# Optimization experiments

Measured on AMD Instinct MI355X. Metric: run time of the kernel, lower is better.

The kernel has to match this reference:

```python
import jax, jax.numpy as jnp
import numpy as np

D, H, HKV, HD = 1024, 16, 4, 64
GQ = H // HKV           # query heads per kv head (gqa_groups)
BS, STRIDE, TB, WIN = 32, 16, 16, 512
NEG = -1e9
EPS = 1e-5


def _ln(x, w, b):
    m = x.mean(-1, keepdims=True)
    v = ((x - m) ** 2).mean(-1, keepdims=True)
    return (x - m) * jax.lax.rsqrt(v + EPS) * w + b


def setup_inputs():
    key = jax.random.key(0)
    ks = jax.random.split(key, 20)
    B, S = 2, 2048
    w = lambda k, s: jax.random.normal(k, s, jnp.float32) * 0.02
    return dict(
        x=jax.random.normal(ks[0], (B, S, D), jnp.float32),
        ln1_w=jnp.ones((D,), jnp.float32), ln1_b=jnp.zeros((D,), jnp.float32),
        wq=w(ks[1], (D, H * HD)), bq=jnp.zeros((H * HD,), jnp.float32),
        wk=w(ks[2], (D, HKV * HD)), bk=jnp.zeros((HKV * HD,), jnp.float32),
        wv=w(ks[3], (D, HKV * HD)), bv=jnp.zeros((HKV * HD,), jnp.float32),
        wg=w(ks[4], (D, 3 * H)), bg=jnp.zeros((3 * H,), jnp.float32),
        wo=w(ks[5], (H * HD, D)), bo=jnp.zeros((D,), jnp.float32),
        ln2_w=jnp.ones((D,), jnp.float32), ln2_b=jnp.zeros((D,), jnp.float32),
        w1=w(ks[6], (D, 4 * D)), b1=jnp.zeros((4 * D,), jnp.float32),
        w2=w(ks[7], (4 * D, D)), b2=jnp.zeros((D,), jnp.float32),
    )


def _forward(x, ln1_w, ln1_b, wq, bq, wk, bk, wv, bv, wg, bg, wo, bo,
             ln2_w, ln2_b, w1, b1, w2, b2):
    B, S, _ = x.shape
    nb = S // BS
    h = _ln(x, ln1_w, ln1_b)
    q = (h @ wq + bq).reshape(B, S, H, HD).transpose(0, 2, 1, 3)    # [B,H,S,hd]
    k = (h @ wk + bk).reshape(B, S, HKV, HD).transpose(0, 2, 1, 3)  # [B,Hkv,S,hd]
    v = (h @ wv + bv).reshape(B, S, HKV, HD).transpose(0, 2, 1, 3)
    qg = q.reshape(B, HKV, GQ, S, HD)          # group queries by kv head
    qb = qg.reshape(B, HKV, GQ, nb, BS, HD)    # query blocks
    scale = HD ** -0.5

    # ---- branch 1: compressed attention (overlapping block pooling, stride)
    nc = (S - BS) // STRIDE + 1
    cidx = jnp.arange(nc)[:, None] * STRIDE + jnp.arange(BS)[None, :]
    ck = k[:, :, cidx].mean(axis=3)            # [B,Hkv,nc,hd]
    cv = v[:, :, cidx].mean(axis=3)
    cend = jnp.arange(nc) * STRIDE + BS - 1
    cmask = jnp.arange(S)[:, None] >= cend[None, :]   # [S,nc] causal at block end
    cs = jnp.where(cmask, jnp.einsum('bkgsd,bknd->bkgsn', qg, ck) * scale, NEG)
    oc = jnp.einsum('bkgsn,bknd->bkgsd', jax.nn.softmax(cs, axis=-1), cv)
    oc = jnp.where(cmask.any(-1)[:, None], oc, 0.0)   # zero rows with no visible block

    # ---- branch 2: top-k selected-block attention (selection per query block, per GQA group)
    kbm = k.reshape(B, HKV, nb, BS, HD).mean(3)       # pooled key blocks
    qbm = qb.mean(4)                                  # pooled query blocks
    imp = jnp.einsum('bkgnd,bkmd->bknm', qbm, kbm)    # importance, summed over group heads
    causal_blk = jnp.arange(nb)[:, None] >= jnp.arange(nb)[None, :]
    imp = jnp.where(causal_blk, imp, NEG)
    imp = jnp.where(jnp.eye(nb, dtype=bool), 1e9, imp)  # always keep current block
    _, sel = jax.lax.top_k(imp, TB)                     # [B,Hkv,nb,TB]
    L = TB * BS
    sel_pos = (sel[..., None] * BS + jnp.arange(BS)).reshape(B, HKV, nb, L)
    flat = sel_pos.reshape(B, HKV, nb * L)[..., None]
    sk = jnp.take_along_axis(k, flat, axis=2).reshape(B, HKV, nb, L, HD)
    sv = jnp.take_along_axis(v, flat, axis=2).reshape(B, HKV, nb, L, HD)
    qpos = (jnp.arange(nb) * BS)[:, None] + jnp.arange(BS)            # [nb,BS]
    smask = sel_pos[:, :, :, None, :] <= qpos[None, None, :, :, None]  # [B,Hkv,nb,BS,L]
    ss = jnp.where(smask[:, :, None],
                   jnp.einsum('bkgnqd,bknld->bkgnql', qb, sk) * scale, NEG)
    os_ = jnp.einsum('bkgnql,bknld->bkgnqd', jax.nn.softmax(ss, axis=-1), sv)
    os_ = os_.reshape(B, HKV, GQ, S, HD)

    # ---- branch 3: sliding-window attention (blocked gather, no dense SxS)
    widx = (jnp.arange(nb) * BS)[:, None] + jnp.arange(-WIN, BS)[None, :]
    wmask = (widx[:, None, :] >= 0) & (widx[:, None, :] <= qpos[..., None])
    widxc = jnp.clip(widx, 0, S - 1)
    wk_ = k[:, :, widxc]
    wv_ = v[:, :, widxc]
    ws = jnp.where(wmask, jnp.einsum('bkgnqd,bknwd->bkgnqw', qb, wk_) * scale, NEG)
    ow = jnp.einsum('bkgnqw,bknwd->bkgnqd', jax.nn.softmax(ws, axis=-1), wv_)
    ow = ow.reshape(B, HKV, GQ, S, HD)

    # ---- gated combination + output projection
    g = jax.nn.sigmoid(h @ wg + bg).reshape(B, S, H, 3).transpose(0, 2, 1, 3)  # [B,H,S,3]
    att = (g[..., 0:1] * oc.reshape(B, H, S, HD)
           + g[..., 1:2] * os_.reshape(B, H, S, HD)
           + g[..., 2:3] * ow.reshape(B, H, S, HD))
    att = att.transpose(0, 2, 1, 3).reshape(B, S, H * HD) @ wo + bo
    x1 = x + att

    # ---- dense FFN (use_moe=False): Linear -> GELU -> Linear, residual
    h2 = _ln(x1, ln2_w, ln2_b)
    return x1 + jax.nn.gelu(h2 @ w1 + b1, approximate=False) @ w2 + b2


def reference(x, ln1_w, ln1_b, wq, bq, wk, bk, wv, bv, wg, bg, wo, bo,
              ln2_w, ln2_b, w1, b1, w2, b2):
    return _forward(x, ln1_w, ln1_b, wq, bq, wk, bk, wv, bv, wg, bg, wo, bo,
                    ln2_w, ln2_b, w1, b1, w2, b2)
```

## Files before the change

### kernel.cpp

```cpp
#include <hip/hip_runtime.h>
#include <hip/hip_bf16.h>
#include <math.h>

typedef __hip_bfloat16 bft;
typedef __attribute__((ext_vector_type(8))) short bf16x8;
typedef __attribute__((ext_vector_type(4))) float f32x4;

constexpr int cB = 2, cS = 2048, cD = 1024, cH = 16, cHKV = 4, cGQ = 4, cHD = 64;
constexpr int cBS = 32, cTB = 16, cNB = 64, cNC = 127;

#define GL16(gp, lp) __builtin_amdgcn_global_load_lds((const __attribute__((address_space(1))) void*)(gp), (__attribute__((address_space(3))) void*)(lp), 16, 0, 0)
#define FENCE asm volatile("" ::: "memory")

__device__ __forceinline__ float bf2f(short h) {
    return __uint_as_float(((unsigned int)(unsigned short)h) << 16);
}

__global__ void k_transpose_cvt(const float* __restrict__ src, bft* __restrict__ dst, int K, int N) {
    __shared__ float tile[32][33];
    int kb = blockIdx.x * 32, nb = blockIdx.y * 32;
    int tx = threadIdx.x, ty = threadIdx.y;
    #pragma unroll
    for (int i = 0; i < 32; i += 8) {
        int k = kb + ty + i, n = nb + tx;
        tile[ty + i][tx] = (k < K && n < N) ? src[(size_t)k * N + n] : 0.f;
    }
    __syncthreads();
    #pragma unroll
    for (int i = 0; i < 32; i += 8) {
        int n = nb + ty + i, k = kb + tx;
        if (n < N && k < K) dst[(size_t)n * K + k] = __float2bfloat16(tile[tx][ty + i]);
    }
}

__global__ __launch_bounds__(256) void k_ln(const float* __restrict__ src, const float* __restrict__ w,
                                            const float* __restrict__ b, bft* __restrict__ dst) {
    int row = blockIdx.x; int t = threadIdx.x;
    const float4* xr = (const float4*)(src + (size_t)row * cD);
    float4 v = xr[t];
    float s = v.x + v.y + v.z + v.w;
    #pragma unroll
    for (int o = 32; o; o >>= 1) s += __shfl_xor(s, o);
    __shared__ float red[8];
    int wid = t >> 6, lane = t & 63;
    if (lane == 0) red[wid] = s;
    __syncthreads();
    float mean = (red[0] + red[1] + red[2] + red[3]) * (1.f / cD);
    float dx = v.x - mean, dy = v.y - mean, dz = v.z - mean, dw = v.w - mean;
    float sq = dx * dx + dy * dy + dz * dz + dw * dw;
    #pragma unroll
    for (int o = 32; o; o >>= 1) sq += __shfl_xor(sq, o);
    if (lane == 0) red[4 + wid] = sq;
    __syncthreads();
    float var = (red[4] + red[5] + red[6] + red[7]) * (1.f / cD);
    float rstd = rsqrtf(var + 1e-5f);
    float4 wv = ((const float4*)w)[t];
    float4 bv = ((const float4*)b)[t];
    bft* o_ = dst + (size_t)row * cD + t * 4;
    o_[0] = __float2bfloat16(dx * rstd * wv.x + bv.x);
    o_[1] = __float2bfloat16(dy * rstd * wv.y + bv.y);
    o_[2] = __float2bfloat16(dz * rstd * wv.z + bv.z);
    o_[3] = __float2bfloat16(dw * rstd * wv.w + bv.w);
}

template<int MODE>
__global__ __launch_bounds__(256) void k_gemm(const bft* __restrict__ A, const bft* __restrict__ Bt,
        int M, int N, int K,
        const float* __restrict__ bias, const float* __restrict__ add,
        float* __restrict__ outf, bft* __restrict__ outb,
        float* __restrict__ oq, float* __restrict__ okk, float* __restrict__ ovv, float* __restrict__ og,
        const float* __restrict__ bq, const float* __restrict__ bk,
        const float* __restrict__ bv, const float* __restrict__ bg,
        bft* __restrict__ oqb) {
    __shared__ __align__(16) bft As[128 * 64];
    __shared__ __align__(16) bft Bs[128 * 64];
    int tid = threadIdx.x;
    int nwg = gridDim.x * gridDim.y;
    int bid = blockIdx.y * gridDim.x + blockIdx.x;
    int q8 = nwg >> 3;
    int wg = (bid & 7) * q8 + (bid >> 3);
    int bx = wg % gridDim.x, by = wg / gridDim.x;
    int m0 = by * 128, n0 = bx * 128;
    int lane = tid & 63, wid = tid >> 6;
    int wr = wid >> 1, wc = wid & 1;
    int lrow = lane & 15, lk = lane >> 4;
    f32x4 acc[4][4];
    #pragma unroll
    for (int i = 0; i < 4; ++i)
        #pragma unroll
        for (int j = 0; j < 4; ++j) acc[i][j] = (f32x4)0.f;

    for (int kt = 0; kt < K; kt += 64) {
        #pragma unroll
        for (int sh = 0; sh < 4; ++sh) {
            int p = sh * 256 + tid;
            int row = p >> 3;
            int slot = p & 7;
            int ss = slot ^ (row & 7);
            const bft* ga = A + (size_t)(m0 + row) * K + kt + ss * 8;
            const bft* gb = Bt + (size_t)(n0 + row) * K + kt + ss * 8;
            GL16(ga, (char*)As + p * 16);
            GL16(gb, (char*)Bs + p * 16);
        }
        __syncthreads();
        #pragma unroll
        for (int kh = 0; kh < 2; ++kh) {
            bf16x8 af[4], bfv[4];
            #pragma unroll
            for (int mi = 0; mi < 4; ++mi) {
                int row = wr * 64 + mi * 16 + lrow;
                int c8 = kh * 4 + lk;
                af[mi] = *(const bf16x8*)((const char*)As + row * 128 + ((c8 ^ (row & 7)) * 16));
            }
            #pragma unroll
            for (int ni = 0; ni < 4; ++ni) {
                int row = wc * 64 + ni * 16 + lrow;
                int c8 = kh * 4 + lk;
                bfv[ni] = *(const bf16x8*)((const char*)Bs + row * 128 + ((c8 ^ (row & 7)) * 16));
            }
            #pragma unroll
            for (int mi = 0; mi < 4; ++mi)
                #pragma unroll
                for (int ni = 0; ni < 4; ++ni)
                    acc[mi][ni] = __builtin_amdgcn_mfma_f32_16x16x32_bf16(af[mi], bfv[ni], acc[mi][ni], 0, 0, 0);
        }
        __syncthreads();
    }
    #pragma unroll
    for (int mi = 0; mi < 4; ++mi)
        #pragma unroll
        for (int ni = 0; ni < 4; ++ni)
            #pragma unroll
            for (int r = 0; r < 4; ++r) {
                int gr = m0 + wr * 64 + mi * 16 + lk * 4 + r;
                int gc = n0 + wc * 64 + ni * 16 + lrow;
                float val = acc[mi][ni][r];
                if (MODE == 0) {
                    if (gc < 1024) {
                        float qv2 = val + bq[gc];
                        oq[(size_t)gr * 1024 + gc] = qv2;
                        oqb[(size_t)gr * 1024 + gc] = __float2bfloat16(qv2 * 0.125f);
                    }
                    else if (gc < 1280) okk[(size_t)gr * 256 + gc - 1024] = val + bk[gc - 1024];
                    else if (gc < 1536) ovv[(size_t)gr * 256 + gc - 1280] = val + bv[gc - 1280];
                    else if (gc < 1584) {
                        float t2 = val + bg[gc - 1536];
                        og[(size_t)gr * 48 + gc - 1536] = 1.f / (1.f + __expf(-t2));
                    }
                } else if (MODE == 1) {
                    size_t o = (size_t)gr * N + gc;
                    outf[o] = val + bias[gc] + add[o];
                } else if (MODE == 2) {
                    float t2 = val + bias[gc];
                    float ge = 0.5f * t2 * (1.f + erff(t2 * 0.70710678118654752f));
                    outb[(size_t)gr * N + gc] = __float2bfloat16(ge);
                } else {
                    size_t o = (size_t)gr * N + gc;
                    outf[o] = val + bias[gc] + add[o];
                }
            }
}

__global__ __launch_bounds__(512) void k_gemm256_gelu(const bft* __restrict__ A, const bft* __restrict__ Bt,
                                                      const float* __restrict__ bias, bft* __restrict__ outb) {
    constexpr int K = 1024, N = 4096, NT = K / 64;
    __shared__ __align__(16) bft As[2][256 * 64];
    __shared__ __align__(16) bft Bs[2][256 * 64];
    int tid = threadIdx.x;
    int nwg = gridDim.x * gridDim.y;
    int bid = blockIdx.y * gridDim.x + blockIdx.x;
    int q8 = nwg >> 3;
    int wg = (bid & 7) * q8 + (bid >> 3);
    int bx = wg % gridDim.x, by = wg / gridDim.x;
    int m0 = by * 256, n0 = bx * 256;
    int w = tid >> 6, lane = tid & 63, lrow = lane & 15, lk = lane >> 4;
    int wr = w >> 2, wc = w & 3;
    int l8 = lane >> 3, l7 = lane & 7;
    int ssrc = (l7 ^ l8) * 8;

    auto stageA = [&](int buf, int h, int kt) {
        int rbase = 32 * w + 16 * h;
        const bft* g0 = A + (size_t)(m0 + rbase + l8) * K + kt + ssrc;
        GL16(g0, (char*)As[buf] + rbase * 128 + lane * 16);
        const bft* g1 = A + (size_t)(m0 + rbase + 8 + l8) * K + kt + ssrc;
        GL16(g1, (char*)As[buf] + rbase * 128 + 1024 + lane * 16);
    };
    auto stageB = [&](int buf, int h, int kt) {
        int rbase = 32 * w + 16 * h;
        const bft* g0 = Bt + (size_t)(n0 + rbase + l8) * K + kt + ssrc;
        GL16(g0, (char*)Bs[buf] + rbase * 128 + lane * 16);
        const bft* g1 = Bt + (size_t)(n0 + rbase + 8 + l8) * K + kt + ssrc;
        GL16(g1, (char*)Bs[buf] + rbase * 128 + 1024 + lane * 16);
    };
    auto ldA = [&](int buf, int mi, int kk) {
        int r = wr * 128 + mi * 16 + lrow;
        return *(const bf16x8*)((const char*)As[buf] + r * 128 + (((kk * 4 + lk) ^ (r & 7)) * 16));
    };
    auto ldB = [&](int buf, int ni, int kk) {
        int r = wc * 64 + ni * 16 + lrow;
        return *(const bf16x8*)((const char*)Bs[buf] + r * 128 + (((kk * 4 + lk) ^ (r & 7)) * 16));
    };

    f32x4 acc[8][4];
    #pragma unroll
    for (int i = 0; i < 8; ++i)
        #pragma unroll
        for (int j = 0; j < 4; ++j) acc[i][j] = (f32x4)0.f;

    stageA(0, 0, 0); stageB(0, 0, 0); stageA(0, 1, 0); stageB(0, 1, 0);
    asm volatile("s_waitcnt vmcnt(4)" ::: "memory");
    FENCE; __builtin_amdgcn_s_barrier(); FENCE;

    bf16x8 aE[4][2], aO[4][2], bE[2][2], bO[2][2];
    for (int t = 0; t < NT; ++t) {
        int cur = t & 1, nxt = cur ^ 1;
        int ktn = (t + 1) * 64;
        bool pre = (t + 1 < NT);
        #pragma unroll
        for (int i = 0; i < 4; ++i)
            #pragma unroll
            for (int kk = 0; kk < 2; ++kk) aE[i][kk] = ldA(cur, 2 * i, kk);
        #pragma unroll
        for (int j = 0; j < 2; ++j)
            #pragma unroll
            for (int kk = 0; kk < 2; ++kk) bE[j][kk] = ldB(cur, 2 * j, kk);
        if (pre) { stageA(nxt, 0, ktn); asm volatile("s_waitcnt vmcnt(2)" ::: "memory"); }
        else     {                       asm volatile("s_waitcnt vmcnt(0)" ::: "memory"); }
        FENCE; __builtin_amdgcn_s_barrier(); FENCE;
        __builtin_amdgcn_s_setprio(1);
        #pragma unroll
        for (int i = 0; i < 4; ++i)
            #pragma unroll
            for (int j = 0; j < 2; ++j)
                #pragma unroll
                for (int kk = 0; kk < 2; ++kk)
                    acc[2 * i][2 * j] = __builtin_amdgcn_mfma_f32_16x16x32_bf16(aE[i][kk], bE[j][kk], acc[2 * i][2 * j], 0, 0, 0);
        __builtin_amdgcn_s_setprio(0);
        FENCE; __builtin_amdgcn_s_barrier(); FENCE;
        #pragma unroll
        for (int j = 0; j < 2; ++j)
            #pragma unroll
            for (int kk = 0; kk < 2; ++kk) bO[j][kk] = ldB(cur, 2 * j + 1, kk);
        if (pre) stageB(nxt, 0, ktn);
        FENCE; __builtin_amdgcn_s_barrier(); FENCE;
        __builtin_amdgcn_s_setprio(1);
        #pragma unroll
        for (int i = 0; i < 4; ++i)
            #pragma unroll
            for (int j = 0; j < 2; ++j)
                #pragma unroll
                for (int kk = 0; kk < 2; ++kk)
                    acc[2 * i][2 * j + 1] = __builtin_amdgcn_mfma_f32_16x16x32_bf16(aE[i][kk], bO[j][kk], acc[2 * i][2 * j + 1], 0, 0, 0);
        __builtin_amdgcn_s_setprio(0);
        FENCE; __builtin_amdgcn_s_barrier(); FENCE;
        #pragma unroll
        for (int i = 0; i < 4; ++i)
            #pragma unroll
            for (int kk = 0; kk < 2; ++kk) aO[i][kk] = ldA(cur, 2 * i + 1, kk);
        if (pre) stageA(nxt, 1, ktn);
        FENCE; __builtin_amdgcn_s_barrier(); FENCE;
        __builtin_amdgcn_s_setprio(1);
        #pragma unroll
        for (int i = 0; i < 4; ++i)
            #pragma unroll
            for (int j = 0; j < 2; ++j)
                #pragma unroll
                for (int kk = 0; kk < 2; ++kk)
                    acc[2 * i + 1][2 * j] = __builtin_amdgcn_mfma_f32_16x16x32_bf16(aO[i][kk], bE[j][kk], acc[2 * i + 1][2 * j], 0, 0, 0);
        __builtin_amdgcn_s_setprio(0);
        FENCE; __builtin_amdgcn_s_barrier(); FENCE;
        if (pre) { stageB(nxt, 1, ktn); asm volatile("s_waitcnt vmcnt(4)" ::: "memory"); }
        FENCE; __builtin_amdgcn_s_barrier(); FENCE;
        __builtin_amdgcn_s_setprio(1);
        #pragma unroll
        for (int i = 0; i < 4; ++i)
            #pragma unroll
            for (int j = 0; j < 2; ++j)
                #pragma unroll
                for (int kk = 0; kk < 2; ++kk)
                    acc[2 * i + 1][2 * j + 1] = __builtin_amdgcn_mfma_f32_16x16x32_bf16(aO[i][kk], bO[j][kk], acc[2 * i + 1][2 * j + 1], 0, 0, 0);
        __builtin_amdgcn_s_setprio(0);
        FENCE; __builtin_amdgcn_s_barrier(); FENCE;
    }
    #pragma unroll
    for (int mi = 0; mi < 8; ++mi)
        #pragma unroll
        for (int ni = 0; ni < 4; ++ni)
            #pragma unroll
            for (int r = 0; r < 4; ++r) {
                int gr = m0 + wr * 128 + mi * 16 + lk * 4 + r;
                int gc = n0 + wc * 64 + ni * 16 + lrow;
                float t2 = acc[mi][ni][r] + bias[gc];
                float ge = 0.5f * t2 * (1.f + erff(t2 * 0.70710678118654752f));
                outb[(size_t)gr * N + gc] = __float2bfloat16(ge);
            }
}

__global__ __launch_bounds__(512) void k_gemm256_sk(const bft* __restrict__ A, const bft* __restrict__ Bt,
                                                    bft* __restrict__ q0, bft* __restrict__ q1,
                                                    bft* __restrict__ q2, bft* __restrict__ q3) {
    constexpr int KT = 4096, N = 1024, NT = 16;
    __shared__ __align__(16) bft As[2][256 * 64];
    __shared__ __align__(16) bft Bs[2][256 * 64];
    int tid = threadIdx.x;
    int flat = blockIdx.x;
    int wg = (flat & 7) * 32 + (flat >> 3);
    int slice = wg >> 6; int rem = wg & 63;
    int m0 = (rem >> 2) * 256, n0 = (rem & 3) * 256;
    int kbase = slice * 1024;
    int w = tid >> 6, lane = tid & 63, lrow = lane & 15, lk = lane >> 4;
    int wr = w >> 2, wc = w & 3;
    int l8 = lane >> 3, l7 = lane & 7;
    int ssrc = (l7 ^ l8) * 8;

    auto stageA = [&](int buf, int h, int kt) {
        int rbase = 32 * w + 16 * h;
        const bft* g0 = A + (size_t)(m0 + rbase + l8) * KT + kbase + kt + ssrc;
        GL16(g0, (char*)As[buf] + rbase * 128 + lane * 16);
        const bft* g1 = A + (size_t)(m0 + rbase + 8 + l8) * KT + kbase + kt + ssrc;
        GL16(g1, (char*)As[buf] + rbase * 128 + 1024 + lane * 16);
    };
    auto stageB = [&](int buf, int h, int kt) {
        int rbase = 32 * w + 16 * h;
        const bft* g0 = Bt + (size_t)(n0 + rbase + l8) * KT + kbase + kt + ssrc;
        GL16(g0, (char*)Bs[buf] + rbase * 128 + lane * 16);
        const bft* g1 = Bt + (size_t)(n0 + rbase + 8 + l8) * KT + kbase + kt + ssrc;
        GL16(g1, (char*)Bs[buf] + rbase * 128 + 1024 + lane * 16);
    };
    auto ldA = [&](int buf, int mi, int kk) {
        int r = wr * 128 + mi * 16 + lrow;
        return *(const bf16x8*)((const char*)As[buf] + r * 128 + (((kk * 4 + lk) ^ (r & 7)) * 16));
    };
    auto ldB = [&](int buf, int ni, int kk) {
        int r = wc * 64 + ni * 16 + lrow;
        return *(const bf16x8*)((const char*)Bs[buf] + r * 128 + (((kk * 4 + lk) ^ (r & 7)) * 16));
    };

    f32x4 acc[8][4];
    #pragma unroll
    for (int i = 0; i < 8; ++i)
        #pragma unroll
        for (int j = 0; j < 4; ++j) acc[i][j] = (f32x4)0.f;

    stageA(0, 0, 0); stageB(0, 0, 0); stageA(0, 1, 0); stageB(0, 1, 0);
    asm volatile("s_waitcnt vmcnt(4)" ::: "memory");
    FENCE; __builtin_amdgcn_s_barrier(); FENCE;

    bf16x8 aE[4][2], aO[4][2], bE[2][2], bO[2][2];
    for (int t = 0; t < NT; ++t) {
        int cur = t & 1, nxt = cur ^ 1;
        int ktn = (t + 1) * 64;
        bool pre = (t + 1 < NT);
        #pragma unroll
        for (int i = 0; i < 4; ++i)
            #pragma unroll
            for (int kk = 0; kk < 2; ++kk) aE[i][kk] = ldA(cur, 2 * i, kk);
        #pragma unroll
        for (int j = 0; j < 2; ++j)
            #pragma unroll
            for (int kk = 0; kk < 2; ++kk) bE[j][kk] = ldB(cur, 2 * j, kk);
        if (pre) { stageA(nxt, 0, ktn); asm volatile("s_waitcnt vmcnt(2)" ::: "memory"); }
        else     {                       asm volatile("s_waitcnt vmcnt(0)" ::: "memory"); }
        FENCE; __builtin_amdgcn_s_barrier(); FENCE;
        __builtin_amdgcn_s_setprio(1);
        #pragma unroll
        for (int i = 0; i < 4; ++i)
            #pragma unroll
            for (int j = 0; j < 2; ++j)
                #pragma unroll
                for (int kk = 0; kk < 2; ++kk)
                    acc[2 * i][2 * j] = __builtin_amdgcn_mfma_f32_16x16x32_bf16(aE[i][kk], bE[j][kk], acc[2 * i][2 * j], 0, 0, 0);
        __builtin_amdgcn_s_setprio(0);
        FENCE; __builtin_amdgcn_s_barrier(); FENCE;
        #pragma unroll
        for (int j = 0; j < 2; ++j)
            #pragma unroll
            for (int kk = 0; kk < 2; ++kk) bO[j][kk] = ldB(cur, 2 * j + 1, kk);
        if (pre) stageB(nxt, 0, ktn);
        FENCE; __builtin_amdgcn_s_barrier(); FENCE;
        __builtin_amdgcn_s_setprio(1);
        #pragma unroll
        for (int i = 0; i < 4; ++i)
            #pragma unroll
            for (int j = 0; j < 2; ++j)
                #pragma unroll
                for (int kk = 0; kk < 2; ++kk)
                    acc[2 * i][2 * j + 1] = __builtin_amdgcn_mfma_f32_16x16x32_bf16(aE[i][kk], bO[j][kk], acc[2 * i][2 * j + 1], 0, 0, 0);
        __builtin_amdgcn_s_setprio(0);
        FENCE; __builtin_amdgcn_s_barrier(); FENCE;
        #pragma unroll
        for (int i = 0; i < 4; ++i)
            #pragma unroll
            for (int kk = 0; kk < 2; ++kk) aO[i][kk] = ldA(cur, 2 * i + 1, kk);
        if (pre) stageA(nxt, 1, ktn);
        FENCE; __builtin_amdgcn_s_barrier(); FENCE;
        __builtin_amdgcn_s_setprio(1);
        #pragma unroll
        for (int i = 0; i < 4; ++i)
            #pragma unroll
            for (int j = 0; j < 2; ++j)
                #pragma unroll
                for (int kk = 0; kk < 2; ++kk)
                    acc[2 * i + 1][2 * j] = __builtin_amdgcn_mfma_f32_16x16x32_bf16(aO[i][kk], bE[j][kk], acc[2 * i + 1][2 * j], 0, 0, 0);
        __builtin_amdgcn_s_setprio(0);
        FENCE; __builtin_amdgcn_s_barrier(); FENCE;
        if (pre) { stageB(nxt, 1, ktn); asm volatile("s_waitcnt vmcnt(4)" ::: "memory"); }
        FENCE; __builtin_amdgcn_s_barrier(); FENCE;
        __builtin_amdgcn_s_setprio(1);
        #pragma unroll
        for (int i = 0; i < 4; ++i)
            #pragma unroll
            for (int j = 0; j < 2; ++j)
                #pragma unroll
                for (int kk = 0; kk < 2; ++kk)
                    acc[2 * i + 1][2 * j + 1] = __builtin_amdgcn_mfma_f32_16x16x32_bf16(aO[i][kk], bO[j][kk], acc[2 * i + 1][2 * j + 1], 0, 0, 0);
        __builtin_amdgcn_s_setprio(0);
        FENCE; __builtin_amdgcn_s_barrier(); FENCE;
    }
    bft* pp = (slice == 0) ? q0 : (slice == 1) ? q1 : (slice == 2) ? q2 : q3;
    #pragma unroll
    for (int mi = 0; mi < 8; ++mi)
        #pragma unroll
        for (int ni = 0; ni < 4; ++ni)
            #pragma unroll
            for (int r = 0; r < 4; ++r) {
                int gr = m0 + wr * 128 + mi * 16 + lk * 4 + r;
                int gc = n0 + wc * 64 + ni * 16 + lrow;
                pp[(size_t)gr * N + gc] = __float2bfloat16(acc[mi][ni][r]);
            }
}

__global__ __launch_bounds__(256) void k_mlpred(const bft* __restrict__ q0, const bft* __restrict__ q1,
                                                const bft* __restrict__ q2, const bft* __restrict__ q3,
                                                const float* __restrict__ x1, const float* __restrict__ b2,
                                                float* __restrict__ out) {
    size_t i = ((size_t)blockIdx.x * 256 + threadIdx.x) * 8;
    bf16x8 a0 = *(const bf16x8*)(q0 + i);
    bf16x8 a1 = *(const bf16x8*)(q1 + i);
    bf16x8 a2 = *(const bf16x8*)(q2 + i);
    bf16x8 a3 = *(const bf16x8*)(q3 + i);
    int col = (int)(i & 1023);
    float4 b0 = *(const float4*)(b2 + col);
    float4 b1v = *(const float4*)(b2 + col + 4);
    float4 x0 = *(const float4*)(x1 + i);
    float4 x1v = *(const float4*)(x1 + i + 4);
    float s[8];
    #pragma unroll
    for (int j = 0; j < 8; ++j)
        s[j] = bf2f(a0[j]) + bf2f(a1[j]) + bf2f(a2[j]) + bf2f(a3[j]);
    float4 o0 = make_float4(s[0] + b0.x + x0.x, s[1] + b0.y + x0.y, s[2] + b0.z + x0.z, s[3] + b0.w + x0.w);
    float4 o1 = make_float4(s[4] + b1v.x + x1v.x, s[5] + b1v.y + x1v.y, s[6] + b1v.z + x1v.z, s[7] + b1v.w + x1v.w);
    *(float4*)(out + i) = o0;
    *(float4*)(out + i + 4) = o1;
}

__global__ __launch_bounds__(64) void k_cmp_kv(const float* __restrict__ k, const float* __restrict__ v,
                                               bft* __restrict__ ck, bft* __restrict__ cvT) {
    int idx = blockIdx.x;
    int n = idx & 127; int bk = idx >> 7; int kv = bk & 3; int b = bk >> 2;
    int d = threadIdx.x;
    if (n == 127) {
        ck[(size_t)bk * 8192 + 127 * 64 + d] = __float2bfloat16(0.f);
        cvT[(size_t)bk * 8192 + d * 128 + 127] = __float2bfloat16(0.f);
        return;
    }
    float sk = 0.f, sv = 0.f;
    int base = b * cS + n * 16;
    for (int j = 0; j < cBS; ++j) {
        size_t o = (size_t)(base + j) * 256 + kv * 64 + d;
        sk += k[o]; sv += v[o];
    }
    ck[(size_t)bk * 8192 + n * 64 + d] = __float2bfloat16(sk * (1.f / 32.f));
    cvT[(size_t)bk * 8192 + d * 128 + n] = __float2bfloat16(sv * (1.f / 32.f));
}

__global__ __launch_bounds__(256) void k_cmp_attn(const float* __restrict__ q, const bft* __restrict__ ck,
                                                  const bft* __restrict__ cvT, const float* __restrict__ gates,
                                                  float* __restrict__ att) {
    __shared__ __align__(16) bft Qs[256 * 64];
    __shared__ __align__(16) bft Ks[128 * 64];
    __shared__ __align__(16) bft VTs[64 * 128];
    __shared__ __align__(16) bft Ps[4 * 16 * 128];
    int idx = blockIdx.x;
    int chunk = idx & 31; int bk = idx >> 5; int kv = bk & 3; int b = bk >> 2;
    int tid = threadIdx.x;
    {
        int r = tid; int h = r >> 6, toff = r & 63;
        const float4* src = (const float4*)(q + ((size_t)(b * cS + chunk * 64 + toff)) * 1024 + (kv * 4 + h) * 64);
        #pragma unroll
        for (int s = 0; s < 8; ++s) {
            float4 a = src[2 * s], c = src[2 * s + 1];
            bf16x8 pk;
            bft* pe = (bft*)&pk;
            pe[0] = __float2bfloat16(a.x); pe[1] = __float2bfloat16(a.y);
            pe[2] = __float2bfloat16(a.z); pe[3] = __float2bfloat16(a.w);
            pe[4] = __float2bfloat16(c.x); pe[5] = __float2bfloat16(c.y);
            pe[6] = __float2bfloat16(c.z); pe[7] = __float2bfloat16(c.w);
            *(bf16x8*)((char*)Qs + r * 128 + ((s ^ (r & 7)) * 16)) = pk;
        }
    }
    if (tid < 128) {
        int r = tid;
        const bf16x8* src = (const bf16x8*)(ck + (size_t)bk * 8192 + r * 64);
        #pragma unroll
        for (int s = 0; s < 8; ++s)
            *(bf16x8*)((char*)Ks + r * 128 + ((s ^ (r & 7)) * 16)) = src[s];
    }
    if (tid < 64) {
        int r = tid;
        const bf16x8* src = (const bf16x8*)(cvT + (size_t)bk * 8192 + r * 128);
        #pragma unroll
        for (int s = 0; s < 16; ++s)
            *(bf16x8*)((char*)VTs + r * 256 + ((s ^ (r & 7)) * 16)) = src[s];
    }
    __syncthreads();

    int w = tid >> 6, lane = tid & 63, lrow = lane & 15, lk = lane >> 4;
    int hg = kv * cGQ + w;
    #pragma unroll
    for (int rt = 0; rt < 4; ++rt) {
        int rowb = w * 64 + rt * 16;
        bf16x8 aq[2];
        #pragma unroll
        for (int kh = 0; kh < 2; ++kh) {
            int r = rowb + lrow;
            aq[kh] = *(const bf16x8*)((const char*)Qs + r * 128 + (((kh * 4 + lk) ^ (r & 7)) * 16));
        }
        f32x4 sa[8];
        #pragma unroll
        for (int nt = 0; nt < 8; ++nt) {
            sa[nt] = (f32x4)0.f;
            #pragma unroll
            for (int kh = 0; kh < 2; ++kh) {
                int kr = nt * 16 + lrow;
                bf16x8 bv_ = *(const bf16x8*)((const char*)Ks + kr * 128 + (((kh * 4 + lk) ^ (kr & 7)) * 16));
                sa[nt] = __builtin_amdgcn_mfma_f32_16x16x32_bf16(aq[kh], bv_, sa[nt], 0, 0, 0);
            }
        }
        float mrow[4], srow[4]; int nv[4];
        #pragma unroll
        for (int r = 0; r < 4; ++r) {
            int s_abs = chunk * 64 + rt * 16 + lk * 4 + r;
            nv[r] = (s_abs >= 31) ? (((s_abs - 31) >> 4) + 1) : 0;
            mrow[r] = -INFINITY; srow[r] = 0.f;
        }
        #pragma unroll
        for (int nt = 0; nt < 8; ++nt) {
            int key = nt * 16 + lrow;
            #pragma unroll
            for (int r = 0; r < 4; ++r) {
                float sc = sa[nt][r] * 0.125f;
                if (key < nv[r]) mrow[r] = fmaxf(mrow[r], sc);
            }
        }
        #pragma unroll
        for (int r = 0; r < 4; ++r) {
            #pragma unroll
            for (int o = 8; o; o >>= 1) mrow[r] = fmaxf(mrow[r], __shfl_xor(mrow[r], o));
        }
        #pragma unroll
        for (int nt = 0; nt < 8; ++nt) {
            int key = nt * 16 + lrow;
            #pragma unroll
            for (int r = 0; r < 4; ++r) {
                float sc = sa[nt][r] * 0.125f;
                float p = (key < nv[r]) ? __expf(sc - mrow[r]) : 0.f;
                srow[r] += p;
                int rit = lk * 4 + r;
                *(bft*)((char*)Ps + w * 4096 + rit * 256 + ((((key >> 3) ^ (rit & 7))) * 16) + (key & 7) * 2) =
                    __float2bfloat16(p);
            }
        }
        #pragma unroll
        for (int r = 0; r < 4; ++r) {
            #pragma unroll
            for (int o = 8; o; o >>= 1) srow[r] += __shfl_xor(srow[r], o);
        }
        f32x4 oa[4];
        #pragma unroll
        for (int dt = 0; dt < 4; ++dt) oa[dt] = (f32x4)0.f;
        #pragma unroll
        for (int kc = 0; kc < 4; ++kc) {
            bf16x8 pa = *(const bf16x8*)((const char*)Ps + w * 4096 + lrow * 256 + (((kc * 4 + lk) ^ (lrow & 7)) * 16));
            #pragma unroll
            for (int dt = 0; dt < 4; ++dt) {
                int vr = dt * 16 + lrow;
                bf16x8 vb = *(const bf16x8*)((const char*)VTs + vr * 256 + (((kc * 4 + lk) ^ (vr & 7)) * 16));
                oa[dt] = __builtin_amdgcn_mfma_f32_16x16x32_bf16(pa, vb, oa[dt], 0, 0, 0);
            }
        }
        float inv[4]; int toks[4];
        #pragma unroll
        for (int r = 0; r < 4; ++r) {
            int tok = chunk * 64 + rt * 16 + lk * 4 + r;
            toks[r] = tok;
            float g0 = gates[((size_t)(b * cS + tok)) * 48 + hg * 3 + 0];
            inv[r] = (srow[r] > 0.f) ? (g0 / srow[r]) : 0.f;
        }
        #pragma unroll
        for (int dt = 0; dt < 4; ++dt)
            #pragma unroll
            for (int r = 0; r < 4; ++r)
                att[((size_t)(b * cS + toks[r])) * 1024 + hg * 64 + dt * 16 + lrow] = oa[dt][r] * inv[r];
    }
}

__global__ __launch_bounds__(256) void k_kvprep(const float* __restrict__ k, const float* __restrict__ v,
                                                bft* __restrict__ kb16, bft* __restrict__ vT16) {
    __shared__ float vt[64 * 65];
    int idx = blockIdx.x; int tc = idx & 31; int kv = (idx >> 5) & 3; int b = idx >> 7;
    int t = threadIdx.x; int ti = t >> 2, seg = t & 3, d0 = seg * 16;
    const float4* ks = (const float4*)(k + (size_t)(b * cS + tc * 64 + ti) * 256 + kv * 64 + d0);
    const float4* vs = (const float4*)(v + (size_t)(b * cS + tc * 64 + ti) * 256 + kv * 64 + d0);
    bft* kd = kb16 + ((size_t)(b * 4 + kv) * 2048 + tc * 64 + ti) * 64 + d0;
    #pragma unroll
    for (int i = 0; i < 4; ++i) {
        float4 a = ks[i];
        kd[i * 4 + 0] = __float2bfloat16(a.x); kd[i * 4 + 1] = __float2bfloat16(a.y);
        kd[i * 4 + 2] = __float2bfloat16(a.z); kd[i * 4 + 3] = __float2bfloat16(a.w);
        float4 c = vs[i];
        vt[ti * 65 + d0 + i * 4 + 0] = c.x; vt[ti * 65 + d0 + i * 4 + 1] = c.y;
        vt[ti * 65 + d0 + i * 4 + 2] = c.z; vt[ti * 65 + d0 + i * 4 + 3] = c.w;
    }
    __syncthreads();
    int d = t >> 2, ts0 = (t & 3) * 16;
    bft* vd = vT16 + ((size_t)(b * 4 + kv) * 64 + d) * 2048 + tc * 64 + ts0;
    #pragma unroll
    for (int i = 0; i < 16; ++i) vd[i] = __float2bfloat16(vt[(ts0 + i) * 65 + d]);
}

__global__ __launch_bounds__(256) void k_selwin(const bft* __restrict__ qb16, const bft* __restrict__ kb16,
                                                const bft* __restrict__ vT16, const int* __restrict__ sel,
                                                const float* __restrict__ gates, const float* __restrict__ attb,
                                                bft* __restrict__ att16) {
    __shared__ __align__(16) bft Qs[128 * 64];
    __shared__ __align__(16) bft Ks[3][32 * 64];
    __shared__ __align__(16) bft Vs[3][64 * 32];
    __shared__ __align__(16) bft Ps[4][32 * 32];
    __shared__ int msL[40];
    __shared__ int nmS[2];
    int idx = blockIdx.x;
    int n = idx & 63; int kv = (idx >> 6) & 3; int b = idx >> 8;
    int bkv = b * 4 + kv;
    int tid = threadIdx.x;
    int w = tid >> 6, lane = tid & 63, lrow = lane & 15, lk = lane >> 4;
    int h = kv * 4 + w;

    #pragma unroll
    for (int c = 0; c < 4; ++c) {
        int p = c * 256 + tid; int r = p >> 3, s = p & 7;
        const bft* src = qb16 + ((size_t)(b * cS + n * 32 + (r & 31))) * 1024 + (kv * 4 + (r >> 5)) * 64 + ((s ^ (r & 7)) * 8);
        GL16(src, (char*)Qs + p * 16);
    }
    {
        int p = tid; int row = p >> 3, s = p & 7;
        const bft* srck = kb16 + ((size_t)bkv * 2048 + n * 32 + row) * 64 + ((s ^ (row & 7)) * 8);
        GL16(srck, (char*)Ks[0] + p * 16);
        int rowv = p >> 2, g3 = p & 3;
        const bft* srcv = vT16 + ((size_t)bkv * 64 + rowv) * 2048 + n * 32 + ((g3 ^ (rowv & 3)) * 8);
        GL16(srcv, (char*)Vs[0] + p * 16);
    }
    if (tid == 0) {
        const int* selp = sel + ((size_t)bkv * cNB + n) * cTB;
        int nm = 0;
        #pragma unroll
        for (int t = 0; t < cTB; ++t) { int m = selp[t]; if (m <= n) msL[nm++] = m; }
        nmS[0] = nm;
        int m0 = (n > 16) ? (n - 16) : 0;
        for (int m = m0; m <= n; ++m) msL[nm++] = m;
        nmS[1] = nm;
    }
    asm volatile("s_waitcnt vmcnt(0)" ::: "memory");
    FENCE; __builtin_amdgcn_s_barrier(); FENCE;

    int p1 = nmS[0], nm = nmS[1];
    bf16x8 qf[2][2];
    #pragma unroll
    for (int qt = 0; qt < 2; ++qt)
        #pragma unroll
        for (int kh = 0; kh < 2; ++kh) {
            int r = w * 32 + qt * 16 + lrow;
            qf[qt][kh] = *(const bf16x8*)((const char*)Qs + r * 128 + (((kh * 4 + lk) ^ (r & 7)) * 16));
        }

    f32x4 oa[2][4], accf[2][4];
    float sacc[2] = {0.f, 0.f};
    #pragma unroll
    for (int qt = 0; qt < 2; ++qt)
        #pragma unroll
        for (int dt = 0; dt < 4; ++dt) { oa[qt][dt] = (f32x4)0.f; accf[qt][dt] = (f32x4)0.f; }

    for (int i = 0; i < nm; ++i) {
        int buf = i % 3;
        if (i == 0 && nm > 1) {
            int m1 = msL[1];
            int p = tid; int row = p >> 3, s = p & 7;
            const bft* srck = kb16 + ((size_t)bkv * 2048 + m1 * 32 + row) * 64 + ((s ^ (row & 7)) * 8);
            GL16(srck, (char*)Ks[1] + p * 16);
            int rowv = p >> 2, g3 = p & 3;
            const bft* srcv = vT16 + ((size_t)bkv * 64 + rowv) * 2048 + m1 * 32 + ((g3 ^ (rowv & 3)) * 8);
            GL16(srcv, (char*)Vs[1] + p * 16);
        }
        if (i + 2 < nm) {
            int m2 = msL[i + 2]; int sl = (i + 2) % 3;
            int p = tid; int row = p >> 3, s = p & 7;
            const bft* srck = kb16 + ((size_t)bkv * 2048 + m2 * 32 + row) * 64 + ((s ^ (row & 7)) * 8);
            GL16(srck, (char*)Ks[sl] + p * 16);
            int rowv = p >> 2, g3 = p & 3;
            const bft* srcv = vT16 + ((size_t)bkv * 64 + rowv) * 2048 + m2 * 32 + ((g3 ^ (rowv & 3)) * 8);
            GL16(srcv, (char*)Vs[sl] + p * 16);
        }
        int m = msL[i];
        bool diag = (m == n);
        #pragma unroll
        for (int qt = 0; qt < 2; ++qt) {
            int q = qt * 16 + lrow;
            #pragma unroll
            for (int kt = 0; kt < 2; ++kt) {
                f32x4 a = (f32x4)0.f;
                #pragma unroll
                for (int kh = 0; kh < 2; ++kh) {
                    int kr = kt * 16 + lrow;
                    bf16x8 ak = *(const bf16x8*)((const char*)Ks[buf] + kr * 128 + (((kh * 4 + lk) ^ (kr & 7)) * 16));
                    a = __builtin_amdgcn_mfma_f32_16x16x32_bf16(ak, qf[qt][kh], a, 0, 0, 0);
                }
                int k0 = kt * 16 + lk * 4;
                float p0 = (!diag || k0 <= q)     ? __expf(a[0]) : 0.f;
                float p1v = (!diag || k0 + 1 <= q) ? __expf(a[1]) : 0.f;
                float p2 = (!diag || k0 + 2 <= q) ? __expf(a[2]) : 0.f;
                float p3 = (!diag || k0 + 3 <= q) ? __expf(a[3]) : 0.f;
                sacc[qt] += p0 + p1v + p2 + p3;
                bft h0 = __float2bfloat16(p0), h1 = __float2bfloat16(p1v);
                bft h2 = __float2bfloat16(p2), h3 = __float2bfloat16(p3);
                unsigned int w0 = ((unsigned int)(*(unsigned short*)&h1) << 16) | (unsigned int)(*(unsigned short*)&h0);
                unsigned int w1 = ((unsigned int)(*(unsigned short*)&h3) << 16) | (unsigned int)(*(unsigned short*)&h2);
                int g = kt * 2 + (lk >> 1);
                *(uint2*)((char*)Ps[w] + q * 64 + ((g ^ (q & 3)) * 16) + (lk & 1) * 8) = make_uint2(w0, w1);
            }
        }
        #pragma unroll
        for (int qt = 0; qt < 2; ++qt) {
            int q = qt * 16 + lrow;
            bf16x8 pa = *(const bf16x8*)((const char*)Ps[w] + q * 64 + ((lk ^ (q & 3)) * 16));
            #pragma unroll
            for (int dt = 0; dt < 4; ++dt) {
                int vr = dt * 16 + lrow;
                bf16x8 vb = *(const bf16x8*)((const char*)Vs[buf] + vr * 64 + ((lk ^ (vr & 3)) * 16));
                oa[qt][dt] = __builtin_amdgcn_mfma_f32_16x16x32_bf16(pa, vb, oa[qt][dt], 0, 0, 0);
            }
        }
        if (i == p1 - 1 || i == nm - 1) {
            int gi = (i == p1 - 1) ? 1 : 2;
            #pragma unroll
            for (int qt = 0; qt < 2; ++qt) {
                float s2 = sacc[qt];
                s2 += __shfl_xor(s2, 16); s2 += __shfl_xor(s2, 32);
                #pragma unroll
                for (int r = 0; r < 4; ++r) {
                    float l = __shfl(s2, lk * 4 + r);
                    int tok = n * 32 + qt * 16 + lk * 4 + r;
                    float g = gates[((size_t)(b * cS + tok)) * 48 + h * 3 + gi];
                    float f = g / l;
                    #pragma unroll
                    for (int dt = 0; dt < 4; ++dt) accf[qt][dt][r] += f * oa[qt][dt][r];
                }
                sacc[qt] = 0.f;
                #pragma unroll
                for (int dt = 0; dt < 4; ++dt) oa[qt][dt] = (f32x4)0.f;
            }
        }
        if (i + 1 < nm) {
            if (i + 2 < nm) { asm volatile("s_waitcnt vmcnt(2)" ::: "memory"); }
            else            { asm volatile("s_waitcnt vmcnt(0)" ::: "memory"); }
            FENCE; __builtin_amdgcn_s_barrier(); FENCE;
        }
    }
    #pragma unroll
    for (int qt = 0; qt < 2; ++qt)
        #pragma unroll
        for (int dt = 0; dt < 4; ++dt)
            #pragma unroll
            for (int r = 0; r < 4; ++r) {
                int tok = n * 32 + qt * 16 + lk * 4 + r;
                size_t a_ = ((size_t)(b * cS + tok)) * 1024 + h * 64 + dt * 16 + lrow;
                att16[a_] = __float2bfloat16(attb[a_] + accf[qt][dt][r]);
            }
}

__global__ __launch_bounds__(64) void k_blockmeans(const float* __restrict__ k, const float* __restrict__ q,
                                                   float* __restrict__ kbm, float* __restrict__ qs) {
    int idx = blockIdx.x; int m = idx & 63; int kvb = idx >> 6; int kv = kvb & 3; int b = kvb >> 2;
    int d = threadIdx.x;
    float sk = 0.f;
    for (int j = 0; j < cBS; ++j) sk += k[(size_t)(b * cS + m * 32 + j) * 256 + kv * 64 + d];
    size_t o = ((size_t)(b * cHKV + kv) * cNB + m) * 64 + d;
    kbm[o] = sk * (1.f / 32.f);
    float sq = 0.f;
    for (int j = 0; j < cBS; ++j) {
        size_t tb = (size_t)(b * cS + m * 32 + j) * 1024 + kv * 256 + d;
        sq += q[tb] + q[tb + 64] + q[tb + 128] + q[tb + 192];
    }
    qs[o] = sq * (1.f / 32.f);
}

__global__ __launch_bounds__(64) void k_topk(const float* __restrict__ qs, const float* __restrict__ kbm,
                                             int* __restrict__ sel) {
    int idx = blockIdx.x; int n = idx & 63; int kvb = idx >> 6; int kv = kvb & 3; int b = kvb >> 2;
    int lane = threadIdx.x;
    __shared__ float qrow[64];
    size_t base = (size_t)(b * cHKV + kv) * cNB;
    qrow[lane] = qs[(base + n) * 64 + lane];
    __syncthreads();
    float val;
    if (lane <= n) {
        const float* kb = kbm + (base + lane) * 64;
        float s_ = 0.f;
        for (int d = 0; d < 64; ++d) s_ += qrow[d] * kb[d];
        val = (lane == n) ? 1e9f : s_;
    } else val = -1e9f;
    int* so = sel + (base + n) * cTB;
    float v_ = val;
    for (int t = 0; t < cTB; ++t) {
        float bv = v_; int bi = lane;
        #pragma unroll
        for (int o = 32; o; o >>= 1) {
            float ov = __shfl_xor(bv, o); int oi = __shfl_xor(bi, o);
            if (ov > bv || (ov == bv && oi < bi)) { bv = ov; bi = oi; }
        }
        if (lane == 0) so[t] = bi;
        if (lane == bi) v_ = -INFINITY;
    }
}

extern "C" void kernel_launch(void* const* d_in, const int* in_sizes, int n_in,
                              void* d_out, int out_size, void* d_ws, size_t ws_size,
                              hipStream_t stream) {
    const float* x    = (const float*)d_in[0];
    const float* ln1w = (const float*)d_in[1];
    const float* ln1b = (const float*)d_in[2];
    const float* wq   = (const float*)d_in[3];
    const float* bq   = (const float*)d_in[4];
    const float* wk   = (const float*)d_in[5];
    const float* bk   = (const float*)d_in[6];
    const float* wv   = (const float*)d_in[7];
    const float* bv   = (const float*)d_in[8];
    const float* wg   = (const float*)d_in[9];
    const float* bg   = (const float*)d_in[10];
    const float* wo   = (const float*)d_in[11];
    const float* bo   = (const float*)d_in[12];
    const float* ln2w = (const float*)d_in[13];
    const float* ln2b = (const float*)d_in[14];
    const float* w1   = (const float*)d_in[15];
    const float* b1   = (const float*)d_in[16];
    const float* w2   = (const float*)d_in[17];
    const float* b2   = (const float*)d_in[18];

    char* ws = (char*)d_ws;
    const size_t MiB = 1024 * 1024;
    bft*  wcatT = (bft*) (ws);
    bft*  woT   = (bft*) (ws + 3 * MiB + 256 * 1024);
    bft*  w1T   = (bft*) (ws + 5 * MiB + 256 * 1024);
    bft*  w2T   = (bft*) (ws + 13 * MiB + 256 * 1024);
    bft*  hbuf  = (bft*) (ws + 21 * MiB + 256 * 1024);
    float* qbuf = (float*)(ws + 29 * MiB + 256 * 1024);
    float* kbuf = (float*)(ws + 45 * MiB + 256 * 1024);
    float* vbuf = (float*)(ws + 49 * MiB + 256 * 1024);
    float* gbuf = (float*)(ws + 53 * MiB + 256 * 1024);
    bft*  ckb   = (bft*)  (ws + 55 * MiB + 256 * 1024);
    bft*  cvTb  = (bft*)  (ws + 56 * MiB + 256 * 1024);
    float* kbmb = (float*)(ws + 57 * MiB + 256 * 1024);
    float* qsb  = (float*)(ws + 57 * MiB + 384 * 1024);
    int*   selb = (int*)  (ws + 57 * MiB + 512 * 1024);
    float* attb = (float*)(ws + 58 * MiB);
    bft*  att16 = (bft*) (ws + 74 * MiB);
    float* x1b  = (float*)(ws + 82 * MiB);
    bft*  zbuf  = (bft*) (ws + 29 * MiB + 256 * 1024);
    bft*  kb16  = (bft*) (ws + 21 * MiB + 256 * 1024);
    bft*  vT16  = (bft*) (ws + 23 * MiB + 256 * 1024);
    bft*  qb16  = (bft*) (ws + 82 * MiB);
    bft*  skp0  = (bft*) (ws);
    bft*  skp1  = (bft*) (ws + 21 * MiB + 256 * 1024);
    bft*  skp2  = (bft*) (ws + 61 * MiB + 256 * 1024);
    bft*  skp3  = (bft*) (ws + 69 * MiB + 256 * 1024);

    dim3 t328(32, 8);
    k_transpose_cvt<<<dim3(32, 32), t328, 0, stream>>>(wq, wcatT, 1024, 1024);
    k_transpose_cvt<<<dim3(32, 8),  t328, 0, stream>>>(wk, wcatT + (size_t)1024 * 1024, 1024, 256);
    k_transpose_cvt<<<dim3(32, 8),  t328, 0, stream>>>(wv, wcatT + (size_t)1280 * 1024, 1024, 256);
    k_transpose_cvt<<<dim3(32, 2),  t328, 0, stream>>>(wg, wcatT + (size_t)1536 * 1024, 1024, 48);
    hipMemsetAsync(wcatT + (size_t)1584 * 1024, 0, (size_t)80 * 1024 * 2, stream);
    k_transpose_cvt<<<dim3(32, 32), t328, 0, stream>>>(wo, woT, 1024, 1024);
    k_transpose_cvt<<<dim3(32, 128), t328, 0, stream>>>(w1, w1T, 1024, 4096);
    k_transpose_cvt<<<dim3(128, 32), t328, 0, stream>>>(w2, w2T, 4096, 1024);
    k_ln<<<4096, 256, 0, stream>>>(x, ln1w, ln1b, hbuf);
    k_gemm<0><<<dim3(13, 32), 256, 0, stream>>>(hbuf, wcatT, 4096, 1664, 1024,
        nullptr, nullptr, nullptr, nullptr, qbuf, kbuf, vbuf, gbuf, bq, bk, bv, bg, qb16);
    k_kvprep<<<256, 256, 0, stream>>>(kbuf, vbuf, kb16, vT16);
    k_cmp_kv<<<8 * 128, 64, 0, stream>>>(kbuf, vbuf, ckb, cvTb);
    k_cmp_attn<<<256, 256, 0, stream>>>(qbuf, ckb, cvTb, gbuf, attb);
    k_blockmeans<<<cB * cHKV * cNB, 64, 0, stream>>>(kbuf, qbuf, kbmb, qsb);
    k_topk<<<cB * cHKV * cNB, 64, 0, stream>>>(qsb, kbmb, selb);
    k_selwin<<<512, 256, 0, stream>>>(qb16, kb16, vT16, selb, gbuf, attb, att16);
    k_gemm<1><<<dim3(8, 32), 256, 0, stream>>>(att16, woT, 4096, 1024, 1024,
        bo, x, x1b, nullptr, nullptr, nullptr, nullptr, nullptr, nullptr, nullptr, nullptr, nullptr, nullptr);
    k_ln<<<4096, 256, 0, stream>>>(x1b, ln2w, ln2b, hbuf);
    k_gemm256_gelu<<<dim3(16, 16), 512, 0, stream>>>(hbuf, w1T, b1, zbuf);
    k_gemm256_sk<<<256, 512, 0, stream>>>(zbuf, w2T, skp0, skp1, skp2, skp3);
    k_mlpred<<<2048, 256, 0, stream>>>(skp0, skp1, skp2, skp3, x1b, b2, (float*)d_out);
}
```

Before: 318.3 us.

## Issue all next-tile LDS prefetches up front and remap GEMM tiles per XCD

In both 256x256 bf16 GEMM kernels, all four global-to-LDS stage loads for the next K tile are now issued together at the start of each iteration, instead of being spread across the four MFMA phases. The vmcnt waits are adjusted to match, so the even-half tiles are ready by the end of the iteration and the odd halves by the next wait. The aim is to give the global loads longer to complete behind compute. The GELU GEMM also replaces the generic XCD swizzle with a fixed mapping that gives each XCD a contiguous 8x4 block of output tiles, to improve L2 reuse. That mapping assumes a 16x16 grid, and issuing everything early concentrates memory traffic at the start of each iteration.

```diff
diff --git a/kernel.cpp b/kernel.cpp
--- a/kernel.cpp
+++ b/kernel.cpp
@@ -167,11 +167,10 @@
     __shared__ __align__(16) bft As[2][256 * 64];
     __shared__ __align__(16) bft Bs[2][256 * 64];
     int tid = threadIdx.x;
-    int nwg = gridDim.x * gridDim.y;
     int bid = blockIdx.y * gridDim.x + blockIdx.x;
-    int q8 = nwg >> 3;
-    int wg = (bid & 7) * q8 + (bid >> 3);
-    int bx = wg % gridDim.x, by = wg / gridDim.x;
+    int xcd = bid & 7, j = bid >> 3;
+    int by = (xcd >> 2) * 8 + (j >> 2);
+    int bx = (xcd & 3) * 4 + (j & 3);
     int m0 = by * 256, n0 = bx * 256;
     int w = tid >> 6, lane = tid & 63, lrow = lane & 15, lk = lane >> 4;
     int wr = w >> 2, wc = w & 3;
@@ -205,7 +204,7 @@
     #pragma unroll
     for (int i = 0; i < 8; ++i)
         #pragma unroll
-        for (int j = 0; j < 4; ++j) acc[i][j] = (f32x4)0.f;
+        for (int jj = 0; jj < 4; ++jj) acc[i][jj] = (f32x4)0.f;
 
     stageA(0, 0, 0); stageB(0, 0, 0); stageA(0, 1, 0); stageB(0, 1, 0);
     asm volatile("s_waitcnt vmcnt(4)" ::: "memory");
@@ -221,64 +220,66 @@
             #pragma unroll
             for (int kk = 0; kk < 2; ++kk) aE[i][kk] = ldA(cur, 2 * i, kk);
         #pragma unroll
-        for (int j = 0; j < 2; ++j)
-            #pragma unroll
-            for (int kk = 0; kk < 2; ++kk) bE[j][kk] = ldB(cur, 2 * j, kk);
-        if (pre) { stageA(nxt, 0, ktn); asm volatile("s_waitcnt vmcnt(2)" ::: "memory"); }
-        else     {                       asm volatile("s_waitcnt vmcnt(0)" ::: "memory"); }
+        for (int jj = 0; jj < 2; ++jj)
+            #pragma unroll
+            for (int kk = 0; kk < 2; ++kk) bE[jj][kk] = ldB(cur, 2 * jj, kk);
+        if (pre) {
+            stageA(nxt, 0, ktn); stageB(nxt, 0, ktn); stageA(nxt, 1, ktn); stageB(nxt, 1, ktn);
+            asm volatile("s_waitcnt vmcnt(8)" ::: "memory");
+        } else {
+            asm volatile("s_waitcnt vmcnt(0)" ::: "memory");
+        }
         FENCE; __builtin_amdgcn_s_barrier(); FENCE;
         __builtin_amdgcn_s_setprio(1);
         #pragma unroll
         for (int i = 0; i < 4; ++i)
             #pragma unroll
-            for (int j = 0; j < 2; ++j)
+            for (int jj = 0; jj < 2; ++jj)
                 #pragma unroll
                 for (int kk = 0; kk < 2; ++kk)
-                    acc[2 * i][2 * j] = __builtin_amdgcn_mfma_f32_16x16x32_bf16(aE[i][kk], bE[j][kk], acc[2 * i][2 * j], 0, 0, 0);
+                    acc[2 * i][2 * jj] = __builtin_amdgcn_mfma_f32_16x16x32_bf16(aE[i][kk], bE[jj][kk], acc[2 * i][2 * jj], 0, 0, 0);
         __builtin_amdgcn_s_setprio(0);
         FENCE; __builtin_amdgcn_s_barrier(); FENCE;
         #pragma unroll
-        for (int j = 0; j < 2; ++j)
-            #pragma unroll
-            for (int kk = 0; kk < 2; ++kk) bO[j][kk] = ldB(cur, 2 * j + 1, kk);
-        if (pre) stageB(nxt, 0, ktn);
+        for (int jj = 0; jj < 2; ++jj)
+            #pragma unroll
+            for (int kk = 0; kk < 2; ++kk) bO[jj][kk] = ldB(cur, 2 * jj + 1, kk);
         FENCE; __builtin_amdgcn_s_barrier(); FENCE;
         __builtin_amdgcn_s_setprio(1);
         #pragma unroll
         for (int i = 0; i < 4; ++i)
             #pragma unroll
-            for (int j = 0; j < 2; ++j)
+            for (int jj = 0; jj < 2; ++jj)
                 #pragma unroll
                 for (int kk = 0; kk < 2; ++kk)
-                    acc[2 * i][2 * j + 1] = __builtin_amdgcn_mfma_f32_16x16x32_bf16(aE[i][kk], bO[j][kk], acc[2 * i][2 * j + 1], 0, 0, 0);
+                    acc[2 * i][2 * jj + 1] = __builtin_amdgcn_mfma_f32_16x16x32_bf16(aE[i][kk], bO[jj][kk], acc[2 * i][2 * jj + 1], 0, 0, 0);
         __builtin_amdgcn_s_setprio(0);
         FENCE; __builtin_amdgcn_s_barrier(); FENCE;
         #pragma unroll
         for (int i = 0; i < 4; ++i)
             #pragma unroll
             for (int kk = 0; kk < 2; ++kk) aO[i][kk] = ldA(cur, 2 * i + 1, kk);
-        if (pre) stageA(nxt, 1, ktn);
         FENCE; __builtin_amdgcn_s_barrier(); FENCE;
         __builtin_amdgcn_s_setprio(1);
         #pragma unroll
         for (int i = 0; i < 4; ++i)
             #pragma unroll
-            for (int j = 0; j < 2; ++j)
+            for (int jj = 0; jj < 2; ++jj)
                 #pragma unroll
                 for (int kk = 0; kk < 2; ++kk)
-                    acc[2 * i + 1][2 * j] = __builtin_amdgcn_mfma_f32_16x16x32_bf16(aO[i][kk], bE[j][kk], acc[2 * i + 1][2 * j], 0, 0, 0);
+                    acc[2 * i + 1][2 * jj] = __builtin_amdgcn_mfma_f32_16x16x32_bf16(aO[i][kk], bE[jj][kk], acc[2 * i + 1][2 * jj], 0, 0, 0);
         __builtin_amdgcn_s_setprio(0);
         FENCE; __builtin_amdgcn_s_barrier(); FENCE;
-        if (pre) { stageB(nxt, 1, ktn); asm volatile("s_waitcnt vmcnt(4)" ::: "memory"); }
+        if (pre) { asm volatile("s_waitcnt vmcnt(4)" ::: "memory"); }
         FENCE; __builtin_amdgcn_s_barrier(); FENCE;
         __builtin_amdgcn_s_setprio(1);
         #pragma unroll
         for (int i = 0; i < 4; ++i)
             #pragma unroll
-            for (int j = 0; j < 2; ++j)
+            for (int jj = 0; jj < 2; ++jj)
                 #pragma unroll
                 for (int kk = 0; kk < 2; ++kk)
-                    acc[2 * i + 1][2 * j + 1] = __builtin_amdgcn_mfma_f32_16x16x32_bf16(aO[i][kk], bO[j][kk], acc[2 * i + 1][2 * j + 1], 0, 0, 0);
+                    acc[2 * i + 1][2 * jj + 1] = __builtin_amdgcn_mfma_f32_16x16x32_bf16(aO[i][kk], bO[jj][kk], acc[2 * i + 1][2 * jj + 1], 0, 0, 0);
         __builtin_amdgcn_s_setprio(0);
         FENCE; __builtin_amdgcn_s_barrier(); FENCE;
     }
@@ -340,7 +341,7 @@
     #pragma unroll
     for (int i = 0; i < 8; ++i)
         #pragma unroll
-        for (int j = 0; j < 4; ++j) acc[i][j] = (f32x4)0.f;
+        for (int jj = 0; jj < 4; ++jj) acc[i][jj] = (f32x4)0.f;
 
     stageA(0, 0, 0); stageB(0, 0, 0); stageA(0, 1, 0); stageB(0, 1, 0);
     asm volatile("s_waitcnt vmcnt(4)" ::: "memory");
@@ -356,64 +357,66 @@
             #pragma unroll
             for (int kk = 0; kk < 2; ++kk) aE[i][kk] = ldA(cur, 2 * i, kk);
         #pragma unroll
-        for (int j = 0; j < 2; ++j)
-            #pragma unroll
-            for (int kk = 0; kk < 2; ++kk) bE[j][kk] = ldB(cur, 2 * j, kk);
-        if (pre) { stageA(nxt, 0, ktn); asm volatile("s_waitcnt vmcnt(2)" ::: "memory"); }
-        else     {                       asm volatile("s_waitcnt vmcnt(0)" ::: "memory"); }
+        for (int jj = 0; jj < 2; ++jj)
+            #pragma unroll
+            for (int kk = 0; kk < 2; ++kk) bE[jj][kk] = ldB(cur, 2 * jj, kk);
+        if (pre) {
+            stageA(nxt, 0, ktn); stageB(nxt, 0, ktn); stageA(nxt, 1, ktn); stageB(nxt, 1, ktn);
+            asm volatile("s_waitcnt vmcnt(8)" ::: "memory");
+        } else {
+            asm volatile("s_waitcnt vmcnt(0)" ::: "memory");
+        }
         FENCE; __builtin_amdgcn_s_barrier(); FENCE;
         __builtin_amdgcn_s_setprio(1);
         #pragma unroll
         for (int i = 0; i < 4; ++i)
             #pragma unroll
-            for (int j = 0; j < 2; ++j)
+            for (int jj = 0; jj < 2; ++jj)
                 #pragma unroll
                 for (int kk = 0; kk < 2; ++kk)
-                    acc[2 * i][2 * j] = __builtin_amdgcn_mfma_f32_16x16x32_bf16(aE[i][kk], bE[j][kk], acc[2 * i][2 * j], 0, 0, 0);
+                    acc[2 * i][2 * jj] = __builtin_amdgcn_mfma_f32_16x16x32_bf16(aE[i][kk], bE[jj][kk], acc[2 * i][2 * jj], 0, 0, 0);
         __builtin_amdgcn_s_setprio(0);
         FENCE; __builtin_amdgcn_s_barrier(); FENCE;
         #pragma unroll
-        for (int j = 0; j < 2; ++j)
-            #pragma unroll
-            for (int kk = 0; kk < 2; ++kk) bO[j][kk] = ldB(cur, 2 * j + 1, kk);
-        if (pre) stageB(nxt, 0, ktn);
+        for (int jj = 0; jj < 2; ++jj)
+            #pragma unroll
+            for (int kk = 0; kk < 2; ++kk) bO[jj][kk] = ldB(cur, 2 * jj + 1, kk);
         FENCE; __builtin_amdgcn_s_barrier(); FENCE;
         __builtin_amdgcn_s_setprio(1);
         #pragma unroll
         for (int i = 0; i < 4; ++i)
             #pragma unroll
-            for (int j = 0; j < 2; ++j)
+            for (int jj = 0; jj < 2; ++jj)
                 #pragma unroll
                 for (int kk = 0; kk < 2; ++kk)
-                    acc[2 * i][2 * j + 1] = __builtin_amdgcn_mfma_f32_16x16x32_bf16(aE[i][kk], bO[j][kk], acc[2 * i][2 * j + 1], 0, 0, 0);
+                    acc[2 * i][2 * jj + 1] = __builtin_amdgcn_mfma_f32_16x16x32_bf16(aE[i][kk], bO[jj][kk], acc[2 * i][2 * jj + 1], 0, 0, 0);
         __builtin_amdgcn_s_setprio(0);
         FENCE; __builtin_amdgcn_s_barrier(); FENCE;
         #pragma unroll
         for (int i = 0; i < 4; ++i)
             #pragma unroll
             for (int kk = 0; kk < 2; ++kk) aO[i][kk] = ldA(cur, 2 * i + 1, kk);
-        if (pre) stageA(nxt, 1, ktn);
         FENCE; __builtin_amdgcn_s_barrier(); FENCE;
         __builtin_amdgcn_s_setprio(1);
         #pragma unroll
         for (int i = 0; i < 4; ++i)
             #pragma unroll
-            for (int j = 0; j < 2; ++j)
+            for (int jj = 0; jj < 2; ++jj)
                 #pragma unroll
                 for (int kk = 0; kk < 2; ++kk)
-                    acc[2 * i + 1][2 * j] = __builtin_amdgcn_mfma_f32_16x16x32_bf16(aO[i][kk], bE[j][kk], acc[2 * i + 1][2 * j], 0, 0, 0);
+                    acc[2 * i + 1][2 * jj] = __builtin_amdgcn_mfma_f32_16x16x32_bf16(aO[i][kk], bE[jj][kk], acc[2 * i + 1][2 * jj], 0, 0, 0);
         __builtin_amdgcn_s_setprio(0);
         FENCE; __builtin_amdgcn_s_barrier(); FENCE;
-        if (pre) { stageB(nxt, 1, ktn); asm volatile("s_waitcnt vmcnt(4)" ::: "memory"); }
+        if (pre) { asm volatile("s_waitcnt vmcnt(4)" ::: "memory"); }
         FENCE; __builtin_amdgcn_s_barrier(); FENCE;
         __builtin_amdgcn_s_setprio(1);
         #pragma unroll
         for (int i = 0; i < 4; ++i)
             #pragma unroll
-            for (int j = 0; j < 2; ++j)
+            for (int jj = 0; jj < 2; ++jj)
                 #pragma unroll
                 for (int kk = 0; kk < 2; ++kk)
-                    acc[2 * i + 1][2 * j + 1] = __builtin_amdgcn_mfma_f32_16x16x32_bf16(aO[i][kk], bO[j][kk], acc[2 * i + 1][2 * j + 1], 0, 0, 0);
+                    acc[2 * i + 1][2 * jj + 1] = __builtin_amdgcn_mfma_f32_16x16x32_bf16(aO[i][kk], bO[jj][kk], acc[2 * i + 1][2 * jj + 1], 0, 0, 0);
         __builtin_amdgcn_s_setprio(0);
         FENCE; __builtin_amdgcn_s_barrier(); FENCE;
     }
@@ -446,8 +449,8 @@
     float4 x1v = *(const float4*)(x1 + i + 4);
     float s[8];
     #pragma unroll
-    for (int j = 0; j < 8; ++j)
-        s[j] = bf2f(a0[j]) + bf2f(a1[j]) + bf2f(a2[j]) + bf2f(a3[j]);
+    for (int jj = 0; jj < 8; ++jj)
+        s[jj] = bf2f(a0[jj]) + bf2f(a1[jj]) + bf2f(a2[jj]) + bf2f(a3[jj]);
     float4 o0 = make_float4(s[0] + b0.x + x0.x, s[1] + b0.y + x0.y, s[2] + b0.z + x0.z, s[3] + b0.w + x0.w);
     float4 o1 = make_float4(s[4] + b1v.x + x1v.x, s[5] + b1v.y + x1v.y, s[6] + b1v.z + x1v.z, s[7] + b1v.w + x1v.w);
     *(float4*)(out + i) = o0;
```

Result: slower. 327.5 us (+2.9%).
